# Optimization experiments

Hardware: AMD Instinct MI355X
Metric: run time of the kernel (lower is better)

Reference implementation:

```python
import jax, jax.numpy as jnp
import numpy as np

EPS = 1e-05  # matches torch module default eps
B, F = 32768, 1024


def setup_inputs() -> dict:
    key = jax.random.key(0)
    x = jax.random.normal(key, (B, F), dtype=jnp.float32)
    M = jnp.zeros((F,), jnp.float32)  # running mean buffer (_M), _n = 0 at init
    S = jnp.zeros((F,), jnp.float32)  # running M2 buffer (_S)
    return {"x": x, "M": M, "S": S}


def _welford(M, S, x):
    """Sequential Welford update over the batch dim, exactly mirroring push()."""
    def step(carry, xi):
        M, S, n = carry
        n1 = n
        n = n + 1
        nf = n.astype(xi.dtype)
        delta = xi - M
        first = n == 1  # first sample ever: M <- x, S unchanged
        M_new = jnp.where(first, xi, M + delta / nf)
        S_new = jnp.where(first, S, S + delta * delta * (n1.astype(xi.dtype) / nf))
        return (M_new, S_new, n), None

    (M, S, n), _ = jax.lax.scan(step, (M, S, jnp.int32(0)), x)
    return M, S, n


def reference(x, M, S):
    M, S, n = _welford(M, S, x)
    nf = n.astype(x.dtype)
    # var = S / (n - 1) if n > 1 else M**2  (module's .var property)
    var = jnp.where(n > 1, S / (nf - 1.0), jnp.square(M))
    # running stats are requires_grad=False buffers in torch -> constants
    mean = jax.lax.stop_gradient(M)
    std = jax.lax.stop_gradient(jnp.sqrt(var))
    return (x - mean) / (std + EPS)
```

## Files before the change

kernel.cpp:

```cpp
#include <hip/hip_runtime.h>
#include <math.h>

#define NFEAT 1024
#define NROWS 32768
#define EPS 1e-5f

#define NB1 1024
#define RPB1 (NROWS / NB1)
#define FG (NFEAT / 4)
#define NB2 FG
#define NB3 2048
#define RPB3 (NROWS / NB3)

typedef float f32x4 __attribute__((ext_vector_type(4)));


__global__ __launch_bounds__(256) void reduce1_kernel(
    const float* __restrict__ x, f32x4* __restrict__ ps, f32x4* __restrict__ pq)
{
    const int t = threadIdx.x;
    const size_t base = (size_t)(blockIdx.x * RPB1) * FG + t;
    const f32x4* xv = (const f32x4*)x;

    f32x4 s = {0.f, 0.f, 0.f, 0.f};
    f32x4 q = {0.f, 0.f, 0.f, 0.f};

    #pragma unroll
    for (int r = 0; r < RPB1; r += 4) {
        f32x4 v0 = xv[base + (size_t)(r + 0) * FG];
        f32x4 v1 = xv[base + (size_t)(r + 1) * FG];
        f32x4 v2 = xv[base + (size_t)(r + 2) * FG];
        f32x4 v3 = xv[base + (size_t)(r + 3) * FG];
        s += (v0 + v1) + (v2 + v3);
        q += (v0 * v0 + v1 * v1) + (v2 * v2 + v3 * v3);
    }
    ps[(size_t)blockIdx.x * FG + t] = s;
    pq[(size_t)blockIdx.x * FG + t] = q;
}

__global__ __launch_bounds__(256) void reduce2_kernel(
    const f32x4* __restrict__ ps, const f32x4* __restrict__ pq,
    f32x4* __restrict__ mean, f32x4* __restrict__ inv)
{
    const int t = threadIdx.x;
    const int cgi = blockIdx.x;

    f32x4 s = {0.f, 0.f, 0.f, 0.f};
    f32x4 q = {0.f, 0.f, 0.f, 0.f};
    #pragma unroll
    for (int k = 0; k < NB1 / 256; ++k) {
        s += ps[(size_t)(t + 256 * k) * FG + cgi];
        q += pq[(size_t)(t + 256 * k) * FG + cgi];
    }

    __shared__ f32x4 ls[256];
    __shared__ f32x4 lq[256];
    ls[t] = s; lq[t] = q;
    __syncthreads();
    #pragma unroll
    for (int off = 128; off > 0; off >>= 1) {
        if (t < off) {
            ls[t] += ls[t + off];
            lq[t] += lq[t + off];
        }
        __syncthreads();
    }

    if (t == 0) {
        f32x4 S = ls[0], Q = lq[0];
        const float n   = (float)NROWS;
        const float rn  = 1.0f / n;
        const float rn1 = 1.0f / (n - 1.0f);
        f32x4 m = S * rn, iv;
        iv.x = 1.0f / (sqrtf((Q.x - S.x * S.x * rn) * rn1) + EPS);
        iv.y = 1.0f / (sqrtf((Q.y - S.y * S.y * rn) * rn1) + EPS);
        iv.z = 1.0f / (sqrtf((Q.z - S.z * S.z * rn) * rn1) + EPS);
        iv.w = 1.0f / (sqrtf((Q.w - S.w * S.w * rn) * rn1) + EPS);
        mean[cgi] = m;
        inv[cgi]  = iv;
    }
}

__global__ __launch_bounds__(256) void norm_kernel(
    const float* __restrict__ x,
    const f32x4* __restrict__ mean, const f32x4* __restrict__ inv,
    float* __restrict__ out)
{
    const int t = threadIdx.x;
    const size_t base = (size_t)(blockIdx.x * RPB3) * FG + t;
    const f32x4* xv = (const f32x4*)x;
    f32x4* ov = (f32x4*)out;

    const f32x4 m  = mean[t];
    const f32x4 iv = inv[t];

    #pragma unroll
    for (int r = 0; r < RPB3; r += 4) {
        f32x4 v0 = xv[base + (size_t)(r + 0) * FG];
        f32x4 v1 = xv[base + (size_t)(r + 1) * FG];
        f32x4 v2 = xv[base + (size_t)(r + 2) * FG];
        f32x4 v3 = xv[base + (size_t)(r + 3) * FG];
        ov[base + (size_t)(r + 0) * FG] = (v0 - m) * iv;
        ov[base + (size_t)(r + 1) * FG] = (v1 - m) * iv;
        ov[base + (size_t)(r + 2) * FG] = (v2 - m) * iv;
        ov[base + (size_t)(r + 3) * FG] = (v3 - m) * iv;
    }
}

extern "C" void kernel_launch(void* const* d_in, const int* in_sizes, int n_in,
                              void* d_out, int out_size, void* d_ws, size_t ws_size,
                              hipStream_t stream) {
    const float* x = (const float*)d_in[0];
    float* out = (float*)d_out;

    f32x4* mean = (f32x4*)d_ws;
    f32x4* inv  = mean + FG;
    f32x4* ps   = inv + FG;
    f32x4* pq   = ps + (size_t)NB1 * FG;

    reduce1_kernel<<<NB1, 256, 0, stream>>>(x, ps, pq);
    reduce2_kernel<<<NB2, 256, 0, stream>>>(ps, pq, mean, inv);
    norm_kernel<<<NB3, 256, 0, stream>>>(x, mean, inv, out);
}
```

Baseline: 266.8 us.

## Fuse reduce, finalize and normalize into one persistent kernel with grid barriers

Replaces the three kernel launches with a single kernel of 1024 blocks that computes per-block partial sums, synchronises through atomic-counter grid barriers, finalises mean and inverse std in 256 blocks, then normalises. The second pass re-reads each block's own rows shortly after the first pass, so they may still be in cache (128 KB per block), and two launch gaps are removed. The risks are deadlock if not all 1024 blocks are co-resident (occupancy is hinted at 4 blocks per CU), the cost of barrier spinning, and an extra memset launch.

```diff
diff --git a/kernel.cpp b/kernel.cpp
--- a/kernel.cpp
+++ b/kernel.cpp
@@ -5,105 +5,104 @@
 #define NROWS 32768
 #define EPS 1e-5f
 
-#define NB1 1024
-#define RPB1 (NROWS / NB1)
+#define NB 1024
+#define RPB (NROWS / NB)
 #define FG (NFEAT / 4)
-#define NB2 FG
-#define NB3 2048
-#define RPB3 (NROWS / NB3)
 
 typedef float f32x4 __attribute__((ext_vector_type(4)));
 
 
-__global__ __launch_bounds__(256) void reduce1_kernel(
-    const float* __restrict__ x, f32x4* __restrict__ ps, f32x4* __restrict__ pq)
+__device__ __forceinline__ void dev_barrier(unsigned* cnt, unsigned target)
 {
-    const int t = threadIdx.x;
-    const size_t base = (size_t)(blockIdx.x * RPB1) * FG + t;
-    const f32x4* xv = (const f32x4*)x;
-
-    f32x4 s = {0.f, 0.f, 0.f, 0.f};
-    f32x4 q = {0.f, 0.f, 0.f, 0.f};
-
-    #pragma unroll
-    for (int r = 0; r < RPB1; r += 4) {
-        f32x4 v0 = xv[base + (size_t)(r + 0) * FG];
-        f32x4 v1 = xv[base + (size_t)(r + 1) * FG];
-        f32x4 v2 = xv[base + (size_t)(r + 2) * FG];
-        f32x4 v3 = xv[base + (size_t)(r + 3) * FG];
-        s += (v0 + v1) + (v2 + v3);
-        q += (v0 * v0 + v1 * v1) + (v2 * v2 + v3 * v3);
+    __syncthreads();
+    if (threadIdx.x == 0) {
+        __threadfence();
+        __hip_atomic_fetch_add(cnt, 1u, __ATOMIC_ACQ_REL, __HIP_MEMORY_SCOPE_AGENT);
+        while (__hip_atomic_load(cnt, __ATOMIC_ACQUIRE, __HIP_MEMORY_SCOPE_AGENT) < target)
+            __builtin_amdgcn_s_sleep(2);
     }
-    ps[(size_t)blockIdx.x * FG + t] = s;
-    pq[(size_t)blockIdx.x * FG + t] = q;
+    __syncthreads();
 }
 
-__global__ __launch_bounds__(256) void reduce2_kernel(
-    const f32x4* __restrict__ ps, const f32x4* __restrict__ pq,
-    f32x4* __restrict__ mean, f32x4* __restrict__ inv)
-{
-    const int t = threadIdx.x;
-    const int cgi = blockIdx.x;
-
-    f32x4 s = {0.f, 0.f, 0.f, 0.f};
-    f32x4 q = {0.f, 0.f, 0.f, 0.f};
-    #pragma unroll
-    for (int k = 0; k < NB1 / 256; ++k) {
-        s += ps[(size_t)(t + 256 * k) * FG + cgi];
-        q += pq[(size_t)(t + 256 * k) * FG + cgi];
-    }
-
-    __shared__ f32x4 ls[256];
-    __shared__ f32x4 lq[256];
-    ls[t] = s; lq[t] = q;
-    __syncthreads();
-    #pragma unroll
-    for (int off = 128; off > 0; off >>= 1) {
-        if (t < off) {
-            ls[t] += ls[t + off];
-            lq[t] += lq[t + off];
-        }
-        __syncthreads();
-    }
-
-    if (t == 0) {
-        f32x4 S = ls[0], Q = lq[0];
-        const float n   = (float)NROWS;
-        const float rn  = 1.0f / n;
-        const float rn1 = 1.0f / (n - 1.0f);
-        f32x4 m = S * rn, iv;
-        iv.x = 1.0f / (sqrtf((Q.x - S.x * S.x * rn) * rn1) + EPS);
-        iv.y = 1.0f / (sqrtf((Q.y - S.y * S.y * rn) * rn1) + EPS);
-        iv.z = 1.0f / (sqrtf((Q.z - S.z * S.z * rn) * rn1) + EPS);
-        iv.w = 1.0f / (sqrtf((Q.w - S.w * S.w * rn) * rn1) + EPS);
-        mean[cgi] = m;
-        inv[cgi]  = iv;
-    }
-}
-
-__global__ __launch_bounds__(256) void norm_kernel(
+__global__ __launch_bounds__(256, 4) void fused_kernel(
     const float* __restrict__ x,
-    const f32x4* __restrict__ mean, const f32x4* __restrict__ inv,
+    f32x4* __restrict__ ps, f32x4* __restrict__ pq,
+    f32x4* __restrict__ mean, f32x4* __restrict__ inv,
+    unsigned* __restrict__ bar,
     float* __restrict__ out)
 {
     const int t = threadIdx.x;
-    const size_t base = (size_t)(blockIdx.x * RPB3) * FG + t;
+    const size_t base = (size_t)(blockIdx.x * RPB) * FG + t;
     const f32x4* xv = (const f32x4*)x;
-    f32x4* ov = (f32x4*)out;
 
-    const f32x4 m  = mean[t];
-    const f32x4 iv = inv[t];
+    {
+        f32x4 s = {0.f, 0.f, 0.f, 0.f};
+        f32x4 q = {0.f, 0.f, 0.f, 0.f};
+        #pragma unroll
+        for (int r = 0; r < RPB; r += 4) {
+            f32x4 v0 = xv[base + (size_t)(r + 0) * FG];
+            f32x4 v1 = xv[base + (size_t)(r + 1) * FG];
+            f32x4 v2 = xv[base + (size_t)(r + 2) * FG];
+            f32x4 v3 = xv[base + (size_t)(r + 3) * FG];
+            s += (v0 + v1) + (v2 + v3);
+            q += (v0 * v0 + v1 * v1) + (v2 * v2 + v3 * v3);
+        }
+        ps[(size_t)blockIdx.x * FG + t] = s;
+        pq[(size_t)blockIdx.x * FG + t] = q;
+    }
 
-    #pragma unroll
-    for (int r = 0; r < RPB3; r += 4) {
-        f32x4 v0 = xv[base + (size_t)(r + 0) * FG];
-        f32x4 v1 = xv[base + (size_t)(r + 1) * FG];
-        f32x4 v2 = xv[base + (size_t)(r + 2) * FG];
-        f32x4 v3 = xv[base + (size_t)(r + 3) * FG];
-        ov[base + (size_t)(r + 0) * FG] = (v0 - m) * iv;
-        ov[base + (size_t)(r + 1) * FG] = (v1 - m) * iv;
-        ov[base + (size_t)(r + 2) * FG] = (v2 - m) * iv;
-        ov[base + (size_t)(r + 3) * FG] = (v3 - m) * iv;
+    dev_barrier(&bar[0], NB);
+
+    if (blockIdx.x < FG) {
+        const int cgi = blockIdx.x;
+        f32x4 s = {0.f, 0.f, 0.f, 0.f};
+        f32x4 q = {0.f, 0.f, 0.f, 0.f};
+        #pragma unroll
+        for (int k = 0; k < NB / 256; ++k) {
+            s += ps[(size_t)(t + 256 * k) * FG + cgi];
+            q += pq[(size_t)(t + 256 * k) * FG + cgi];
+        }
+        __shared__ f32x4 ls[256];
+        __shared__ f32x4 lq[256];
+        ls[t] = s; lq[t] = q;
+        __syncthreads();
+        #pragma unroll
+        for (int off = 128; off > 0; off >>= 1) {
+            if (t < off) { ls[t] += ls[t + off]; lq[t] += lq[t + off]; }
+            __syncthreads();
+        }
+        if (t == 0) {
+            f32x4 S = ls[0], Q = lq[0];
+            const float n   = (float)NROWS;
+            const float rn  = 1.0f / n;
+            const float rn1 = 1.0f / (n - 1.0f);
+            f32x4 m = S * rn, iv;
+            iv.x = 1.0f / (sqrtf((Q.x - S.x * S.x * rn) * rn1) + EPS);
+            iv.y = 1.0f / (sqrtf((Q.y - S.y * S.y * rn) * rn1) + EPS);
+            iv.z = 1.0f / (sqrtf((Q.z - S.z * S.z * rn) * rn1) + EPS);
+            iv.w = 1.0f / (sqrtf((Q.w - S.w * S.w * rn) * rn1) + EPS);
+            mean[cgi] = m;
+            inv[cgi]  = iv;
+        }
+    }
+
+    dev_barrier(&bar[1], NB);
+
+    {
+        const f32x4 m  = mean[t];
+        const f32x4 iv = inv[t];
+        f32x4* ov = (f32x4*)out;
+        #pragma unroll
+        for (int r = 0; r < RPB; r += 4) {
+            f32x4 v0 = xv[base + (size_t)(r + 0) * FG];
+            f32x4 v1 = xv[base + (size_t)(r + 1) * FG];
+            f32x4 v2 = xv[base + (size_t)(r + 2) * FG];
+            f32x4 v3 = xv[base + (size_t)(r + 3) * FG];
+            ov[base + (size_t)(r + 0) * FG] = (v0 - m) * iv;
+            ov[base + (size_t)(r + 1) * FG] = (v1 - m) * iv;
+            ov[base + (size_t)(r + 2) * FG] = (v2 - m) * iv;
+            ov[base + (size_t)(r + 3) * FG] = (v3 - m) * iv;
+        }
     }
 }
 
@@ -113,12 +112,16 @@
     const float* x = (const float*)d_in[0];
     float* out = (float*)d_out;
 
-    f32x4* mean = (f32x4*)d_ws;
+    unsigned* bar = (unsigned*)d_ws;
+    f32x4* mean = (f32x4*)((char*)d_ws + 16);
     f32x4* inv  = mean + FG;
     f32x4* ps   = inv + FG;
-    f32x4* pq   = ps + (size_t)NB1 * FG;
+    f32x4* pq   = ps + (size_t)NB * FG;
 
-    reduce1_kernel<<<NB1, 256, 0, stream>>>(x, ps, pq);
-    reduce2_kernel<<<NB2, 256, 0, stream>>>(ps, pq, mean, inv);
-    norm_kernel<<<NB3, 256, 0, stream>>>(x, mean, inv, out);
+    hipMemsetAsync(d_ws, 0, 16, stream);
+
+    void* kargs[] = { (void*)&x, (void*)&ps, (void*)&pq,
+                      (void*)&mean, (void*)&inv, (void*)&bar, (void*)&out };
+    hipLaunchKernel((const void*)fused_kernel, dim3(NB), dim3(256),
+                    kargs, 0, stream);
 }
```

Measured after the change: 524.8 us. 1.97x slower.
